# Performance work log

Measured on AMD Instinct MI355X. Metric: run time of the kernel, lower is better.

## Reference

```python
import jax, jax.numpy as jnp
import numpy as np
import math

HEADS = 16
D_MODEL = 1024
D_K = D_MODEL // HEADS


def setup_inputs() -> dict:
    key = jax.random.key(0)
    ks = jax.random.split(key, 11)
    B, S = 2, 2048
    s = 1.0 / math.sqrt(D_MODEL)
    return {
        "q": jax.random.normal(ks[0], (B, S, D_MODEL), jnp.float32),
        "k": jax.random.normal(ks[1], (B, S, D_MODEL), jnp.float32),
        "v": jax.random.normal(ks[2], (B, S, D_MODEL), jnp.float32),
        "Wq": jax.random.normal(ks[3], (D_MODEL, D_MODEL), jnp.float32) * s,
        "bq": jax.random.normal(ks[4], (D_MODEL,), jnp.float32) * s,
        "Wk": jax.random.normal(ks[5], (D_MODEL, D_MODEL), jnp.float32) * s,
        "bk": jax.random.normal(ks[6], (D_MODEL,), jnp.float32) * s,
        "Wv": jax.random.normal(ks[7], (D_MODEL, D_MODEL), jnp.float32) * s,
        "bv": jax.random.normal(ks[8], (D_MODEL,), jnp.float32) * s,
        "Wo": jax.random.normal(ks[9], (D_MODEL, D_MODEL), jnp.float32) * s,
        "bo": jax.random.normal(ks[10], (D_MODEL,), jnp.float32) * s,
    }


def reference(q, k, v, Wq, bq, Wk, bk, Wv, bv, Wo, bo):
    B, S, _ = q.shape
    # linear projections, split heads: [B, H, S, d_k]
    def proj(x, W, b):
        y = x @ W.T + b
        return y.reshape(B, -1, HEADS, D_K).transpose(0, 2, 1, 3)
    qh, kh, vh = proj(q, Wq, bq), proj(k, Wk, bk), proj(v, Wv, bv)
    # abs-modified scaled dot-product attention (no mask, eval -> no dropout)
    scores = jnp.abs(jnp.einsum("bhsd,bhtd->bhst", qh, kh) / math.sqrt(D_K))
    attn = jax.nn.softmax(scores, axis=-1)
    out = jnp.einsum("bhst,bhtd->bhsd", attn, vh)
    concat = out.transpose(0, 2, 1, 3).reshape(B, S, D_MODEL)
    return concat @ Wo.T + bo
```

## Files before the change

kernel.cpp:

```cpp
#include <hip/hip_runtime.h>

#define HEADS 16
#define DK 64
#define DM 1024
#define SEQ 2048
#define BATCH 2

using bf16x8 = __attribute__((ext_vector_type(8))) short;
using short4v = __attribute__((ext_vector_type(4))) short;
using f32x4 = __attribute__((ext_vector_type(4))) float;

static __device__ __forceinline__ short f2bf(float x) {
  union { float f; unsigned u; } c;
  c.f = x;
  unsigned r = (c.u + 0x7FFFu + ((c.u >> 16) & 1u)) >> 16;
  return (short)r;
}

static __device__ __forceinline__ unsigned pk2bf(float lo, float hi) {
#if __has_builtin(__builtin_amdgcn_cvt_pk_bf16_f32)
  auto t = __builtin_amdgcn_cvt_pk_bf16_f32(lo, hi);
  if constexpr (sizeof(t) == 4) {
    unsigned u;
    __builtin_memcpy(&u, &t, 4);
    return u;
  } else {
    return (unsigned)(unsigned short)f2bf(lo) |
           ((unsigned)(unsigned short)f2bf(hi) << 16);
  }
#else
  return (unsigned)(unsigned short)f2bf(lo) |
         ((unsigned)(unsigned short)f2bf(hi) << 16);
#endif
}

static __device__ __forceinline__ void gload_lds16(const void* g, void* l) {
  __builtin_amdgcn_global_load_lds(
      (const __attribute__((address_space(1))) void*)g,
      (__attribute__((address_space(3))) void*)l, 16, 0, 0);
}

__global__ __launch_bounds__(256) void cvt7(
    const float* __restrict__ s0, const float* __restrict__ s1,
    const float* __restrict__ s2, const float* __restrict__ s3,
    const float* __restrict__ s4, const float* __restrict__ s5,
    const float* __restrict__ s6, short* d0, short* d1, short* d2, short* d3,
    short* d4, short* d5, short* d6) {
  const int y = blockIdx.y;
  const float* s;
  short* d;
  int n;
  switch (y) {
    case 0: s = s0; d = d0; n = BATCH * SEQ * DM; break;
    case 1: s = s1; d = d1; n = BATCH * SEQ * DM; break;
    case 2: s = s2; d = d2; n = BATCH * SEQ * DM; break;
    case 3: s = s3; d = d3; n = DM * DM; break;
    case 4: s = s4; d = d4; n = DM * DM; break;
    case 5: s = s5; d = d5; n = DM * DM; break;
    default: s = s6; d = d6; n = DM * DM; break;
  }
  const int n4 = n >> 2;
  const int stride = gridDim.x * 256;
  for (int i = blockIdx.x * 256 + threadIdx.x; i < n4; i += stride) {
    float4 v = ((const float4*)s)[i];
    uint2 o;
    o.x = pk2bf(v.x, v.y);
    o.y = pk2bf(v.z, v.w);
    ((uint2*)d)[i] = o;
  }
}

__global__ __launch_bounds__(256) void proj_qkv(
    const short* __restrict__ Aq, const short* __restrict__ Ak,
    const short* __restrict__ Av, const short* __restrict__ Wq_,
    const short* __restrict__ Wk_, const short* __restrict__ Wv_,
    const float* __restrict__ bq, const float* __restrict__ bk,
    const float* __restrict__ bv, short* __restrict__ Qh,
    short* __restrict__ Kh, short* __restrict__ Vt) {
  __shared__ short smem[128 * 136];
  short* As = smem;
  short* Ws = smem + 8192;

  const int z = blockIdx.z;
  const short* A = z == 0 ? Aq : z == 1 ? Ak : Av;
  const short* W = z == 0 ? Wq_ : z == 1 ? Wk_ : Wv_;
  const float* bias = z == 0 ? bq : z == 1 ? bk : bv;
  short* C = z == 0 ? Qh : z == 1 ? Kh : Vt;
  const bool tr = (z == 2);

  const int tid = threadIdx.x;
  const int wave = tid >> 6, lane = tid & 63;
  const int quad = lane >> 4, l15 = lane & 15;
  const int n0 = blockIdx.x * 128, m0 = blockIdx.y * 128;
  const int mh = (wave & 1) * 64, nh = (wave >> 1) * 64;
  const int ldr = lane >> 3, ldc = lane & 7;

  f32x4 acc[4][4] = {};

  for (int k0 = 0; k0 < 1024; k0 += 64) {
    __syncthreads();
#pragma unroll
    for (int i = 0; i < 8; ++i) {
      int seg = wave * 8 + i;
      int r = (seg & 15) * 8 + ldr;
      int kb = ldc ^ (r & 7);
      if (seg < 16)
        gload_lds16(&A[(size_t)(m0 + r) * 1024 + k0 + kb * 8], &As[seg * 512]);
      else
        gload_lds16(&W[(size_t)(n0 + r) * 1024 + k0 + kb * 8],
                    &Ws[(seg - 16) * 512]);
    }
    __syncthreads();
#pragma unroll
    for (int ks = 0; ks < 2; ++ks) {
      bf16x8 a[4], b[4];
      int kb = ks * 4 + quad;
#pragma unroll
      for (int f = 0; f < 4; ++f) {
        int rm = mh + f * 16 + l15;
        int rn = nh + f * 16 + l15;
        a[f] = *(const bf16x8*)&As[rm * 64 + (kb ^ (rm & 7)) * 8];
        b[f] = *(const bf16x8*)&Ws[rn * 64 + (kb ^ (rn & 7)) * 8];
      }
#pragma unroll
      for (int mf = 0; mf < 4; ++mf)
#pragma unroll
        for (int nf = 0; nf < 4; ++nf)
          acc[mf][nf] = __builtin_amdgcn_mfma_f32_16x16x32_bf16(
              a[mf], b[nf], acc[mf][nf], 0, 0, 0);
    }
  }

  float bvv[4];
#pragma unroll
  for (int nf = 0; nf < 4; ++nf) bvv[nf] = bias[n0 + nh + nf * 16 + l15];

  __syncthreads();
  short* Cb = smem;

  if (!tr) {
#pragma unroll
    for (int mf = 0; mf < 4; ++mf)
#pragma unroll
      for (int r = 0; r < 4; ++r) {
        int row = mh + mf * 16 + quad * 4 + r;
        unsigned u01 =
            pk2bf(acc[mf][0][r] + bvv[0], acc[mf][1][r] + bvv[1]);
        unsigned u23 =
            pk2bf(acc[mf][2][r] + bvv[2], acc[mf][3][r] + bvv[3]);
        Cb[row * 136 + nh + l15] = (short)u01;
        Cb[row * 136 + nh + 16 + l15] = (short)(u01 >> 16);
        Cb[row * 136 + nh + 32 + l15] = (short)u23;
        Cb[row * 136 + nh + 48 + l15] = (short)(u23 >> 16);
      }
    __syncthreads();
#pragma unroll
    for (int j = 0; j < 8; ++j) {
      int cid = tid + 256 * j;
      int row = cid >> 4, cb = cid & 15;
      bf16x8 v = *(const bf16x8*)&Cb[row * 136 + cb * 8];
      int m = m0 + row, n = n0 + cb * 8;
      int b = m >> 11, s = m & (SEQ - 1), h = n >> 6, d = n & 63;
      *(bf16x8*)&C[((size_t)(b * HEADS + h) * SEQ + s) * DK + d] = v;
    }
  } else {
#pragma unroll
    for (int mf = 0; mf < 4; ++mf)
#pragma unroll
      for (int nf = 0; nf < 4; ++nf)
#pragma unroll
        for (int j = 0; j < 4; ++j) {
          int slot = 16 * quad + 4 * j + mf;
          Cb[(nh + nf * 16 + l15) * 136 + mh + slot] =
              f2bf(acc[mf][nf][j] + bvv[nf]);
        }
    __syncthreads();
#pragma unroll
    for (int j = 0; j < 8; ++j) {
      int cid = tid + 256 * j;
      int row = cid >> 4, cb = cid & 15;
      bf16x8 v = *(const bf16x8*)&Cb[row * 136 + cb * 8];
      int n = n0 + row, m = m0 + cb * 8;
      int b = m >> 11, s = m & (SEQ - 1), h = n >> 6, d = n & 63;
      *(bf16x8*)&C[((size_t)(b * HEADS + h) * DK + d) * SEQ + s] = v;
    }
  }
}

__global__ __launch_bounds__(256) void proj_out(const short* __restrict__ A,
                                                const short* __restrict__ W,
                                                const float* __restrict__ bias,
                                                float* __restrict__ C) {
  __shared__ short smem[12288];
  short* As = smem;
  short* Ws = smem + 8192;

  const int tid = threadIdx.x;
  const int wave = tid >> 6, lane = tid & 63;
  const int quad = lane >> 4, l15 = lane & 15;
  const int n0 = blockIdx.x * 64, m0 = blockIdx.y * 128;
  const int mh = (wave & 1) * 64, nh = (wave >> 1) * 32;
  const int ldr = lane >> 3, ldc = lane & 7;

  f32x4 acc[4][2] = {};

  for (int k0 = 0; k0 < 1024; k0 += 64) {
    __syncthreads();
#pragma unroll
    for (int i = 0; i < 6; ++i) {
      int seg = wave * 6 + i;
      if (seg < 16) {
        int r = seg * 8 + ldr;
        int kb = ldc ^ (r & 7);
        gload_lds16(&A[(size_t)(m0 + r) * 1024 + k0 + kb * 8], &As[seg * 512]);
      } else {
        int r = (seg - 16) * 8 + ldr;
        int kb = ldc ^ (r & 7);
        gload_lds16(&W[(size_t)(n0 + r) * 1024 + k0 + kb * 8],
                    &Ws[(seg - 16) * 512]);
      }
    }
    __syncthreads();
#pragma unroll
    for (int ks = 0; ks < 2; ++ks) {
      bf16x8 a[4], b[2];
      int kb = ks * 4 + quad;
#pragma unroll
      for (int f = 0; f < 4; ++f) {
        int rm = mh + f * 16 + l15;
        a[f] = *(const bf16x8*)&As[rm * 64 + (kb ^ (rm & 7)) * 8];
      }
#pragma unroll
      for (int f = 0; f < 2; ++f) {
        int rn = nh + f * 16 + l15;
        b[f] = *(const bf16x8*)&Ws[rn * 64 + (kb ^ (rn & 7)) * 8];
      }
#pragma unroll
      for (int mf = 0; mf < 4; ++mf)
#pragma unroll
        for (int nf = 0; nf < 2; ++nf)
          acc[mf][nf] = __builtin_amdgcn_mfma_f32_16x16x32_bf16(
              a[mf], b[nf], acc[mf][nf], 0, 0, 0);
    }
  }

  float bvv[2];
#pragma unroll
  for (int nf = 0; nf < 2; ++nf) bvv[nf] = bias[n0 + nh + nf * 16 + l15];
#pragma unroll
  for (int mf = 0; mf < 4; ++mf)
#pragma unroll
    for (int nf = 0; nf < 2; ++nf)
#pragma unroll
      for (int r = 0; r < 4; ++r)
        C[(size_t)(m0 + mh + mf * 16 + quad * 4 + r) * 1024 + n0 + nh +
          nf * 16 + l15] = acc[mf][nf][r] + bvv[nf];
}

__global__ __launch_bounds__(256) void attn_mfma(const short* __restrict__ Qh,
                                                 const short* __restrict__ Kh,
                                                 const short* __restrict__ VtG,
                                                 short* __restrict__ concat) {
  __shared__ short Ks[2][64 * 64];
  __shared__ short Vt[2][64 * 64];
  __shared__ short Ps[128 * 64];

  const int tid = threadIdx.x;
  const int wave = tid >> 6, lane = tid & 63;
  const int quad = lane >> 4, l15 = lane & 15;
  const int bh = blockIdx.y;
  const int q0 = blockIdx.x * 128;
  const size_t base = (size_t)bh * SEQ * DK;
  const int ldr = lane >> 3, ldc = lane & 7;

  bf16x8 qf[2][2];
#pragma unroll
  for (int mf = 0; mf < 2; ++mf)
#pragma unroll
    for (int ks = 0; ks < 2; ++ks)
      qf[mf][ks] =
          *(const bf16x8*)&Qh[base +
                              (size_t)(q0 + wave * 32 + mf * 16 + l15) * 64 +
                              ks * 32 + quad * 8];

  f32x4 O[2][4] = {};
  float lsum[2][4] = {};

  const float CE = 0.18033688011112042f;

#define STAGE_TILE(kt_, b_)                                               \
  {                                                                       \
    _Pragma("unroll") for (int i_ = 0; i_ < 2; ++i_) {                    \
      int seg = wave * 2 + i_;                                            \
      int row = seg * 8 + ldr;                                            \
      int kb = ldc ^ (row & 7);                                           \
      gload_lds16(&Kh[base + (size_t)((kt_)*64 + row) * 64 + kb * 8],     \
                  &Ks[b_][seg * 512]);                                    \
      gload_lds16(&VtG[base + (size_t)row * SEQ + (kt_)*64 + kb * 8],     \
                  &Vt[b_][seg * 512]);                                    \
    }                                                                     \
  }

  STAGE_TILE(0, 0);

  for (int kt = 0; kt < SEQ / 64; ++kt) {
    const int cur = kt & 1;
    __syncthreads();
    if (kt + 1 < SEQ / 64) STAGE_TILE(kt + 1, cur ^ 1);

    f32x4 sf[2][4] = {};
#pragma unroll
    for (int ks = 0; ks < 2; ++ks) {
      bf16x8 bfr[4];
      int kb = ks * 4 + quad;
#pragma unroll
      for (int nf = 0; nf < 4; ++nf) {
        int n = nf * 16 + l15;
        bfr[nf] = *(const bf16x8*)&Ks[cur][n * 64 + (kb ^ (n & 7)) * 8];
      }
#pragma unroll
      for (int mf = 0; mf < 2; ++mf)
#pragma unroll
        for (int nf = 0; nf < 4; ++nf)
          sf[mf][nf] = __builtin_amdgcn_mfma_f32_16x16x32_bf16(
              qf[mf][ks], bfr[nf], sf[mf][nf], 0, 0, 0);
    }

#pragma unroll
    for (int mf = 0; mf < 2; ++mf)
#pragma unroll
      for (int r = 0; r < 4; ++r) {
        float e0 = exp2f(fabsf(sf[mf][0][r]) * CE);
        float e1 = exp2f(fabsf(sf[mf][1][r]) * CE);
        float e2 = exp2f(fabsf(sf[mf][2][r]) * CE);
        float e3 = exp2f(fabsf(sf[mf][3][r]) * CE);
        lsum[mf][r] += (e0 + e1) + (e2 + e3);
        uint2 u;
        u.x = pk2bf(e0, e1);
        u.y = pk2bf(e2, e3);
        int row = wave * 32 + mf * 16 + quad * 4 + r;
        int sw = (row >> 1) & 7;
        int off = (((l15 >> 1) ^ sw) << 3) + 4 * (l15 & 1);
        *(uint2*)&Ps[row * 64 + off] = u;
      }
    __threadfence_block();

#pragma unroll
    for (int ks = 0; ks < 2; ++ks) {
      bf16x8 av[2], bvv[4];
      int kb = ks * 4 + quad;
#pragma unroll
      for (int mf = 0; mf < 2; ++mf) {
        int row = wave * 32 + mf * 16 + l15;
        av[mf] =
            *(const bf16x8*)&Ps[row * 64 + ((kb ^ ((row >> 1) & 7)) << 3)];
      }
#pragma unroll
      for (int nf = 0; nf < 4; ++nf) {
        int n = nf * 16 + l15;
        bvv[nf] = *(const bf16x8*)&Vt[cur][n * 64 + (kb ^ (n & 7)) * 8];
      }
#pragma unroll
      for (int mf = 0; mf < 2; ++mf)
#pragma unroll
        for (int nf = 0; nf < 4; ++nf)
          O[mf][nf] = __builtin_amdgcn_mfma_f32_16x16x32_bf16(
              av[mf], bvv[nf], O[mf][nf], 0, 0, 0);
    }
  }

  float inv[2][4];
#pragma unroll
  for (int mf = 0; mf < 2; ++mf)
#pragma unroll
    for (int r = 0; r < 4; ++r) {
      float s = lsum[mf][r];
#pragma unroll
      for (int x = 1; x < 16; x <<= 1) s += __shfl_xor(s, x, 64);
      inv[mf][r] = 1.f / s;
    }

  __syncthreads();
  const int h2 = l15 >> 3, lo3 = l15 & 7;
#pragma unroll
  for (int mf = 0; mf < 2; ++mf)
#pragma unroll
    for (int nf = 0; nf < 4; ++nf) {
      const int ch = 2 * nf + h2;
#pragma unroll
      for (int r = 0; r < 4; ++r) {
        int row = wave * 32 + mf * 16 + quad * 4 + r;
        float o01 = O[mf][nf][r] * inv[mf][r];
        Ps[row * 64 + ((ch ^ ((row >> 1) & 7)) << 3) + lo3] = f2bf(o01);
      }
    }
  __syncthreads();
  const int b = bh >> 4, h = bh & 15;
#pragma unroll
  for (int j = 0; j < 4; ++j) {
    int cid = tid + 256 * j;
    int row = cid >> 3, cb = cid & 7;
    bf16x8 v = *(const bf16x8*)&Ps[row * 64 + ((cb ^ ((row >> 1) & 7)) << 3)];
    *(bf16x8*)&concat[((size_t)(b * SEQ + q0 + row)) * DM + h * 64 + cb * 8] =
        v;
  }
#undef STAGE_TILE
}

extern "C" void kernel_launch(void* const* d_in, const int* in_sizes, int n_in,
                              void* d_out, int out_size, void* d_ws,
                              size_t ws_size, hipStream_t stream) {
  const float* q = (const float*)d_in[0];
  const float* k = (const float*)d_in[1];
  const float* v = (const float*)d_in[2];
  const float* Wq = (const float*)d_in[3];
  const float* bq = (const float*)d_in[4];
  const float* Wk = (const float*)d_in[5];
  const float* bk = (const float*)d_in[6];
  const float* Wv = (const float*)d_in[7];
  const float* bv = (const float*)d_in[8];
  const float* Wo = (const float*)d_in[9];
  const float* bo = (const float*)d_in[10];

  short* ws = (short*)d_ws;
  const size_t T4 = (size_t)BATCH * SEQ * DM;
  const size_t T1 = (size_t)DM * DM;
  short* qb = ws;
  short* kb_ = ws + T4;
  short* vb = ws + 2 * T4;
  short* Wqb = ws + 3 * T4;
  short* Wkb = Wqb + T1;
  short* Wvb = Wqb + 2 * T1;
  short* Wob = Wqb + 3 * T1;
  short* Qh = Wqb + 4 * T1;
  short* Kh = Qh + T4;
  short* VtG = Qh + 2 * T4;
  short* cc = Qh + 3 * T4;

  cvt7<<<dim3(1024, 7), 256, 0, stream>>>(q, k, v, Wq, Wk, Wv, Wo, qb, kb_, vb,
                                          Wqb, Wkb, Wvb, Wob);

  proj_qkv<<<dim3(DM / 128, (BATCH * SEQ) / 128, 3), 256, 0, stream>>>(
      qb, kb_, vb, Wqb, Wkb, Wvb, bq, bk, bv, Qh, Kh, VtG);

  attn_mfma<<<dim3(SEQ / 128, BATCH * HEADS), 256, 0, stream>>>(Qh, Kh, VtG,
                                                                cc);

  proj_out<<<dim3(DM / 64, (BATCH * SEQ) / 128), 256, 0, stream>>>(
      cc, Wob, bo, (float*)d_out);
}
```

Before: 257.5 us.

## Fuse activation bf16 conversion into QKV projection, single-buffer attention K/V tiles

Removes the separate fp32-to-bf16 pass over q/k/v: proj_qkv now loads fp32 activations directly and converts them into swizzled LDS, while only the weights are pre-converted. The attention kernel drops double-buffered async K/V staging in favour of a single buffer with load-then-sync, which lowers LDS use but exposes load latency. The P and output stores are also rewritten to use packed bf16 conversion with scalar short stores, and the V transpose epilogue uses packed 32-bit LDS writes. Fusing conversion cuts a global round trip of activations, but each projection tile now re-reads fp32 activations once per N-block (8 times).

```diff
diff --git a/kernel.cpp b/kernel.cpp
--- a/kernel.cpp
+++ b/kernel.cpp
@@ -40,26 +40,14 @@
       (__attribute__((address_space(3))) void*)l, 16, 0, 0);
 }
 
-__global__ __launch_bounds__(256) void cvt7(
+__global__ __launch_bounds__(256) void cvt4(
     const float* __restrict__ s0, const float* __restrict__ s1,
-    const float* __restrict__ s2, const float* __restrict__ s3,
-    const float* __restrict__ s4, const float* __restrict__ s5,
-    const float* __restrict__ s6, short* d0, short* d1, short* d2, short* d3,
-    short* d4, short* d5, short* d6) {
+    const float* __restrict__ s2, const float* __restrict__ s3, short* d0,
+    short* d1, short* d2, short* d3) {
   const int y = blockIdx.y;
-  const float* s;
-  short* d;
-  int n;
-  switch (y) {
-    case 0: s = s0; d = d0; n = BATCH * SEQ * DM; break;
-    case 1: s = s1; d = d1; n = BATCH * SEQ * DM; break;
-    case 2: s = s2; d = d2; n = BATCH * SEQ * DM; break;
-    case 3: s = s3; d = d3; n = DM * DM; break;
-    case 4: s = s4; d = d4; n = DM * DM; break;
-    case 5: s = s5; d = d5; n = DM * DM; break;
-    default: s = s6; d = d6; n = DM * DM; break;
-  }
-  const int n4 = n >> 2;
+  const float* s = y == 0 ? s0 : y == 1 ? s1 : y == 2 ? s2 : s3;
+  short* d = y == 0 ? d0 : y == 1 ? d1 : y == 2 ? d2 : d3;
+  const int n4 = (DM * DM) >> 2;
   const int stride = gridDim.x * 256;
   for (int i = blockIdx.x * 256 + threadIdx.x; i < n4; i += stride) {
     float4 v = ((const float4*)s)[i];
@@ -71,8 +59,8 @@
 }
 
 __global__ __launch_bounds__(256) void proj_qkv(
-    const short* __restrict__ Aq, const short* __restrict__ Ak,
-    const short* __restrict__ Av, const short* __restrict__ Wq_,
+    const float* __restrict__ Aq, const float* __restrict__ Ak,
+    const float* __restrict__ Av, const short* __restrict__ Wq_,
     const short* __restrict__ Wk_, const short* __restrict__ Wv_,
     const float* __restrict__ bq, const float* __restrict__ bk,
     const float* __restrict__ bv, short* __restrict__ Qh,
@@ -82,7 +70,7 @@
   short* Ws = smem + 8192;
 
   const int z = blockIdx.z;
-  const short* A = z == 0 ? Aq : z == 1 ? Ak : Av;
+  const float* A = z == 0 ? Aq : z == 1 ? Ak : Av;
   const short* W = z == 0 ? Wq_ : z == 1 ? Wk_ : Wv_;
   const float* bias = z == 0 ? bq : z == 1 ? bk : bv;
   short* C = z == 0 ? Qh : z == 1 ? Kh : Vt;
@@ -100,15 +88,25 @@
   for (int k0 = 0; k0 < 1024; k0 += 64) {
     __syncthreads();
 #pragma unroll
-    for (int i = 0; i < 8; ++i) {
-      int seg = wave * 8 + i;
-      int r = (seg & 15) * 8 + ldr;
+    for (int i = 0; i < 4; ++i) {
+      int seg = wave * 4 + i;
+      int r = seg * 8 + ldr;
       int kb = ldc ^ (r & 7);
-      if (seg < 16)
-        gload_lds16(&A[(size_t)(m0 + r) * 1024 + k0 + kb * 8], &As[seg * 512]);
-      else
-        gload_lds16(&W[(size_t)(n0 + r) * 1024 + k0 + kb * 8],
-                    &Ws[(seg - 16) * 512]);
+      gload_lds16(&W[(size_t)(n0 + r) * 1024 + k0 + kb * 8], &Ws[seg * 512]);
+    }
+#pragma unroll
+    for (int j = 0; j < 4; ++j) {
+      int row = (tid >> 3) + 32 * j;
+      int kb = tid & 7;
+      const float* src = &A[(size_t)(m0 + row) * 1024 + k0 + kb * 8];
+      float4 v0 = *(const float4*)src;
+      float4 v1 = *(const float4*)(src + 4);
+      uint4 u;
+      u.x = pk2bf(v0.x, v0.y);
+      u.y = pk2bf(v0.z, v0.w);
+      u.z = pk2bf(v1.x, v1.y);
+      u.w = pk2bf(v1.z, v1.w);
+      *(uint4*)&As[row * 64 + ((kb ^ (row & 7)) << 3)] = u;
     }
     __syncthreads();
 #pragma unroll
@@ -167,13 +165,15 @@
 #pragma unroll
     for (int mf = 0; mf < 4; ++mf)
 #pragma unroll
-      for (int nf = 0; nf < 4; ++nf)
-#pragma unroll
-        for (int j = 0; j < 4; ++j) {
-          int slot = 16 * quad + 4 * j + mf;
-          Cb[(nh + nf * 16 + l15) * 136 + mh + slot] =
-              f2bf(acc[mf][nf][j] + bvv[nf]);
-        }
+      for (int nf = 0; nf < 4; ++nf) {
+        unsigned u01 =
+            pk2bf(acc[mf][nf][0] + bvv[nf], acc[mf][nf][1] + bvv[nf]);
+        unsigned u23 =
+            pk2bf(acc[mf][nf][2] + bvv[nf], acc[mf][nf][3] + bvv[nf]);
+        int base_ = (nh + nf * 16 + l15) * 136 + mh + mf * 16 + quad * 4;
+        *(unsigned*)&Cb[base_] = u01;
+        *(unsigned*)&Cb[base_ + 2] = u23;
+      }
     __syncthreads();
 #pragma unroll
     for (int j = 0; j < 8; ++j) {
@@ -261,8 +261,8 @@
                                                  const short* __restrict__ Kh,
                                                  const short* __restrict__ VtG,
                                                  short* __restrict__ concat) {
-  __shared__ short Ks[2][64 * 64];
-  __shared__ short Vt[2][64 * 64];
+  __shared__ short Ks[64 * 64];
+  __shared__ short Vt[64 * 64];
   __shared__ short Ps[128 * 64];
 
   const int tid = threadIdx.x;
@@ -288,25 +288,19 @@
 
   const float CE = 0.18033688011112042f;
 
-#define STAGE_TILE(kt_, b_)                                               \
-  {                                                                       \
-    _Pragma("unroll") for (int i_ = 0; i_ < 2; ++i_) {                    \
-      int seg = wave * 2 + i_;                                            \
-      int row = seg * 8 + ldr;                                            \
-      int kb = ldc ^ (row & 7);                                           \
-      gload_lds16(&Kh[base + (size_t)((kt_)*64 + row) * 64 + kb * 8],     \
-                  &Ks[b_][seg * 512]);                                    \
-      gload_lds16(&VtG[base + (size_t)row * SEQ + (kt_)*64 + kb * 8],     \
-                  &Vt[b_][seg * 512]);                                    \
-    }                                                                     \
-  }
-
-  STAGE_TILE(0, 0);
-
   for (int kt = 0; kt < SEQ / 64; ++kt) {
-    const int cur = kt & 1;
-    __syncthreads();
-    if (kt + 1 < SEQ / 64) STAGE_TILE(kt + 1, cur ^ 1);
+    __syncthreads();
+#pragma unroll
+    for (int i = 0; i < 2; ++i) {
+      int seg = wave * 2 + i;
+      int row = seg * 8 + ldr;
+      int kb = ldc ^ (row & 7);
+      gload_lds16(&Kh[base + (size_t)(kt * 64 + row) * 64 + kb * 8],
+                  &Ks[seg * 512]);
+      gload_lds16(&VtG[base + (size_t)row * SEQ + kt * 64 + kb * 8],
+                  &Vt[seg * 512]);
+    }
+    __syncthreads();
 
     f32x4 sf[2][4] = {};
 #pragma unroll
@@ -316,7 +310,7 @@
 #pragma unroll
       for (int nf = 0; nf < 4; ++nf) {
         int n = nf * 16 + l15;
-        bfr[nf] = *(const bf16x8*)&Ks[cur][n * 64 + (kb ^ (n & 7)) * 8];
+        bfr[nf] = *(const bf16x8*)&Ks[n * 64 + (kb ^ (n & 7)) * 8];
       }
 #pragma unroll
       for (int mf = 0; mf < 2; ++mf)
@@ -326,6 +320,7 @@
               qf[mf][ks], bfr[nf], sf[mf][nf], 0, 0, 0);
     }
 
+    const int h2 = l15 >> 3, lo3 = l15 & 7;
 #pragma unroll
     for (int mf = 0; mf < 2; ++mf)
 #pragma unroll
@@ -335,13 +330,15 @@
         float e2 = exp2f(fabsf(sf[mf][2][r]) * CE);
         float e3 = exp2f(fabsf(sf[mf][3][r]) * CE);
         lsum[mf][r] += (e0 + e1) + (e2 + e3);
-        uint2 u;
-        u.x = pk2bf(e0, e1);
-        u.y = pk2bf(e2, e3);
+        unsigned u01 = pk2bf(e0, e1);
+        unsigned u23 = pk2bf(e2, e3);
         int row = wave * 32 + mf * 16 + quad * 4 + r;
         int sw = (row >> 1) & 7;
-        int off = (((l15 >> 1) ^ sw) << 3) + 4 * (l15 & 1);
-        *(uint2*)&Ps[row * 64 + off] = u;
+        short* rp = &Ps[row * 64];
+        rp[(((0 + h2) ^ sw) << 3) + lo3] = (short)u01;
+        rp[(((2 + h2) ^ sw) << 3) + lo3] = (short)(u01 >> 16);
+        rp[(((4 + h2) ^ sw) << 3) + lo3] = (short)u23;
+        rp[(((6 + h2) ^ sw) << 3) + lo3] = (short)(u23 >> 16);
       }
     __threadfence_block();
 
@@ -358,7 +355,7 @@
 #pragma unroll
       for (int nf = 0; nf < 4; ++nf) {
         int n = nf * 16 + l15;
-        bvv[nf] = *(const bf16x8*)&Vt[cur][n * 64 + (kb ^ (n & 7)) * 8];
+        bvv[nf] = *(const bf16x8*)&Vt[n * 64 + (kb ^ (n & 7)) * 8];
       }
 #pragma unroll
       for (int mf = 0; mf < 2; ++mf)
@@ -385,14 +382,16 @@
 #pragma unroll
   for (int mf = 0; mf < 2; ++mf)
 #pragma unroll
-    for (int nf = 0; nf < 4; ++nf) {
-      const int ch = 2 * nf + h2;
-#pragma unroll
-      for (int r = 0; r < 4; ++r) {
-        int row = wave * 32 + mf * 16 + quad * 4 + r;
-        float o01 = O[mf][nf][r] * inv[mf][r];
-        Ps[row * 64 + ((ch ^ ((row >> 1) & 7)) << 3) + lo3] = f2bf(o01);
-      }
+    for (int r = 0; r < 4; ++r) {
+      unsigned u01 = pk2bf(O[mf][0][r] * inv[mf][r], O[mf][1][r] * inv[mf][r]);
+      unsigned u23 = pk2bf(O[mf][2][r] * inv[mf][r], O[mf][3][r] * inv[mf][r]);
+      int row = wave * 32 + mf * 16 + quad * 4 + r;
+      int sw = (row >> 1) & 7;
+      short* rp = &Ps[row * 64];
+      rp[(((0 + h2) ^ sw) << 3) + lo3] = (short)u01;
+      rp[(((2 + h2) ^ sw) << 3) + lo3] = (short)(u01 >> 16);
+      rp[(((4 + h2) ^ sw) << 3) + lo3] = (short)u23;
+      rp[(((6 + h2) ^ sw) << 3) + lo3] = (short)(u23 >> 16);
     }
   __syncthreads();
   const int b = bh >> 4, h = bh & 15;
@@ -404,7 +403,6 @@
     *(bf16x8*)&concat[((size_t)(b * SEQ + q0 + row)) * DM + h * 64 + cb * 8] =
         v;
   }
-#undef STAGE_TILE
 }
 
 extern "C" void kernel_launch(void* const* d_in, const int* in_sizes, int n_in,
@@ -425,10 +423,7 @@
   short* ws = (short*)d_ws;
   const size_t T4 = (size_t)BATCH * SEQ * DM;
   const size_t T1 = (size_t)DM * DM;
-  short* qb = ws;
-  short* kb_ = ws + T4;
-  short* vb = ws + 2 * T4;
-  short* Wqb = ws + 3 * T4;
+  short* Wqb = ws;
   short* Wkb = Wqb + T1;
   short* Wvb = Wqb + 2 * T1;
   short* Wob = Wqb + 3 * T1;
@@ -437,11 +432,10 @@
   short* VtG = Qh + 2 * T4;
   short* cc = Qh + 3 * T4;
 
-  cvt7<<<dim3(1024, 7), 256, 0, stream>>>(q, k, v, Wq, Wk, Wv, Wo, qb, kb_, vb,
-                                          Wqb, Wkb, Wvb, Wob);
+  cvt4<<<dim3(256, 4), 256, 0, stream>>>(Wq, Wk, Wv, Wo, Wqb, Wkb, Wvb, Wob);
 
   proj_qkv<<<dim3(DM / 128, (BATCH * SEQ) / 128, 3), 256, 0, stream>>>(
-      qb, kb_, vb, Wqb, Wkb, Wvb, bq, bk, bv, Qh, Kh, VtG);
+      q, k, v, Wqb, Wkb, Wvb, bq, bk, bv, Qh, Kh, VtG);
 
   attn_mfma<<<dim3(SEQ / 128, BATCH * HEADS), 256, 0, stream>>>(Qh, Kh, VtG,
                                                                 cc);
```

After: 275.5 us. 7.0% more time.
